# Performance work log

Measured on AMD Instinct MI355X. Metric: run time of the kernel, lower is better.

The kernel has to match this reference:

```python
import jax, jax.numpy as jnp
import numpy as np

B, N, D, H = 256, 196, 384, 1536  # batch, patches, dim, mlp hidden


def fake_quant(w, bits):
    """Symmetric per-tensor uniform fake quantization with straight-through estimator."""
    qmax = 2.0 ** (bits - 1) - 1.0
    scale = jnp.maximum(jnp.max(jnp.abs(w)) / qmax, 1e-8)
    q = jnp.clip(jnp.round(w / scale), -qmax, qmax) * scale
    return w + jax.lax.stop_gradient(q - w)


def setup_inputs() -> dict:
    key = jax.random.key(0)
    ks = jax.random.split(key, 8)
    return {
        "x": jax.random.normal(ks[0], (B, N, D), jnp.float32),
        "alpha1": jnp.ones((D,), jnp.float32),
        "beta1": jnp.zeros((D,), jnp.float32),
        "W_attn": jax.random.normal(ks[1], (N, N), jnp.float32) * (1.0 / np.sqrt(N)),
        "b_attn": jnp.zeros((N,), jnp.float32),
        "gamma1": jax.random.uniform(ks[2], (D,), jnp.float32) * 0.1,
        "alpha2": jnp.ones((D,), jnp.float32),
        "beta2": jnp.zeros((D,), jnp.float32),
        "W1": jax.random.normal(ks[3], (H, D), jnp.float32) * (1.0 / np.sqrt(D)),
        "b1": jnp.zeros((H,), jnp.float32),
        "W2": jax.random.normal(ks[4], (D, H), jnp.float32) * (1.0 / np.sqrt(H)),
        "b2": jnp.zeros((D,), jnp.float32),
        "gamma2": jax.random.uniform(ks[5], (D,), jnp.float32) * 0.1,
        "bits": 8,
    }


def reference(x, alpha1, beta1, W_attn, b_attn, gamma1,
              alpha2, beta2, W1, b1, W2, b2, gamma2, bits):
    # --- token-mixing branch ---
    org = x
    h = alpha1 * x + beta1                                   # Aff norm1, [B,N,D]
    # transpose(1,2) -> [B,D,N]; Linear(N,N); transpose back == einsum over patch dim
    Wq = fake_quant(W_attn, bits)
    h = jnp.einsum('bnd,mn->bmd', h, Wq) + b_attn[:, None]   # [B,N,D], bias per patch
    x = gamma1 * h + org                                     # layerscale + residual
    # --- channel-mixing branch ---
    org = x
    h = alpha2 * x + beta2                                   # Aff norm2
    h = jax.nn.gelu(h @ fake_quant(W1, bits).T + b1)         # [B,N,H]
    h = h @ fake_quant(W2, bits).T + b2                      # [B,N,D]
    return gamma2 * h + org
```

## Files before the change

kernel.cpp:

```cpp
#include <hip/hip_runtime.h>
#include <hip/hip_bf16.h>
#include <stdint.h>

#define Bb 256
#define Nn 196
#define Dd 384
#define Hh 1536
#define NPAD 224
#define MPAD 256
#define TTOT (Bb*Nn)
#define XLD 232

typedef __attribute__((ext_vector_type(8))) __bf16 bf16x8;
typedef __attribute__((ext_vector_type(4))) float f32x4;

#define GLD16(gp, lp) __builtin_amdgcn_global_load_lds( \
    (const __attribute__((address_space(1))) void*)(gp), \
    (__attribute__((address_space(3))) void*)(lp), 16, 0, 0)

__device__ __forceinline__ ushort f2bf(float f){
  union { float f; unsigned u; } v; v.f = f;
  unsigned r = v.u + 0x7FFFu + ((v.u >> 16) & 1u);
  return (ushort)(r >> 16);
}

__global__ void absmax_k(const float* __restrict__ w, int n, unsigned* __restrict__ out){
  float m = 0.f;
  for (int i = blockIdx.x*blockDim.x + threadIdx.x; i < n; i += gridDim.x*blockDim.x)
    m = fmaxf(m, fabsf(w[i]));
  #pragma unroll
  for (int o = 32; o >= 1; o >>= 1) m = fmaxf(m, __shfl_xor(m, o));
  __shared__ float sm[4];
  if ((threadIdx.x & 63) == 0) sm[threadIdx.x >> 6] = m;
  __syncthreads();
  if (threadIdx.x == 0){
    float mm = fmaxf(fmaxf(sm[0], sm[1]), fmaxf(sm[2], sm[3]));
    atomicMax(out, __float_as_uint(mm));
  }
}

__global__ void quant_attn_k(const float* __restrict__ W, const unsigned* __restrict__ amax,
                             const int* __restrict__ bitsp, ushort* __restrict__ Wq){
  int idx = blockIdx.x*256 + threadIdx.x;
  int m = idx / NPAD, n = idx - m*NPAD;
  float qmax = (float)((1 << (bitsp[0]-1)) - 1);
  float s = fmaxf(__uint_as_float(amax[0]) / qmax, 1e-8f);
  float v = 0.f;
  if (m < Nn && n < Nn){
    float q = fminf(fmaxf(rintf(W[m*Nn + n] / s), -qmax), qmax);
    v = q * s;
  }
  Wq[idx] = f2bf(v);
}

__global__ void quant_k(const float* __restrict__ W, int n, const unsigned* __restrict__ amax,
                        const int* __restrict__ bitsp, ushort* __restrict__ Wq){
  int idx = blockIdx.x*256 + threadIdx.x;
  if (idx >= n) return;
  float qmax = (float)((1 << (bitsp[0]-1)) - 1);
  float s = fmaxf(__uint_as_float(amax[0]) / qmax, 1e-8f);
  float q = fminf(fmaxf(rintf(W[idx] / s), -qmax), qmax);
  Wq[idx] = f2bf(q * s);
}

__device__ __forceinline__ void stage_tile(const ushort* __restrict__ src, long ld, int k0,
                                           ushort* dst){
  const int tid = threadIdx.x;
  const long row = tid >> 2;
  const int  c8  = (tid & 3) * 8;
  GLD16(src + row*ld + k0 + c8,        dst + tid*8);
  GLD16(src + (row+64)*ld + k0 + c8,   dst + 2048 + tid*8);
}

__device__ __forceinline__ void gemm_core_gl(const ushort* __restrict__ A, long ldA,
                                             const ushort* __restrict__ B, long ldB,
                                             int K, ushort* As, ushort* Bs, f32x4 acc[4][4]){
  const int tid  = threadIdx.x;
  const int lane = tid & 63;
  const int wr   = (tid >> 7) & 1;
  const int wc   = (tid >> 6) & 1;
  const int arow = lane & 15;
  const int koff = (lane >> 4) * 8;
  for (int k0 = 0; k0 < K; k0 += 32){
    __syncthreads();
    stage_tile(A, ldA, k0, As);
    stage_tile(B, ldB, k0, Bs);
    __syncthreads();
    bf16x8 ag[4], bg[4];
    #pragma unroll
    for (int i=0;i<4;i++){
      ag[i] = *(const bf16x8*)&As[(wr*64 + i*16 + arow)*32 + koff];
      bg[i] = *(const bf16x8*)&Bs[(wc*64 + i*16 + arow)*32 + koff];
    }
    #pragma unroll
    for (int i=0;i<4;i++)
      #pragma unroll
      for (int j=0;j<4;j++)
        acc[i][j] = __builtin_amdgcn_mfma_f32_16x16x32_bf16(ag[i], bg[j], acc[i][j], 0, 0, 0);
  }
}

__global__ __launch_bounds__(256) void gemm1_k(const ushort* __restrict__ Wq,
    const float* __restrict__ x,
    const float* __restrict__ alpha1, const float* __restrict__ beta1,
    const float* __restrict__ b_attn, const float* __restrict__ gamma1,
    const float* __restrict__ alpha2, const float* __restrict__ beta2,
    float* __restrict__ x1, ushort* __restrict__ hn2){
  __shared__ ushort Xs[128*XLD];
  __shared__ ushort BufAs[8192];
  const int tid = threadIdx.x;
  const int b = blockIdx.y, dt = blockIdx.x, d0 = dt*128;

  {
    float* buf = (float*)BufAs;
    const int dme = tid & 127;
    const float a1 = alpha1[d0 + dme], be1 = beta1[d0 + dme];
    for (int p = 0; p < 7; p++){
      __syncthreads();
      #pragma unroll
      for (int c = 0; c < 4; c++){
        int nn = p*32 + c*8 + (tid >> 5);
        int ncl = nn < Nn ? nn : Nn - 1;
        GLD16(x + ((long)b*Nn + ncl)*Dd + d0 + (tid & 31)*4,
              (char*)BufAs + c*4096 + tid*16);
      }
      __syncthreads();
      for (int g = tid >> 7; g < 4; g += 2){
        int n0 = g*8;
        ushort o[8];
        #pragma unroll
        for (int t = 0; t < 8; t++){
          int na = p*32 + n0 + t;
          float val = (na < Nn) ? fmaf(a1, buf[(n0 + t)*128 + dme], be1) : 0.f;
          o[t] = f2bf(val);
        }
        *(int4*)&Xs[dme*XLD + p*32 + n0] = *(int4*)o;
      }
    }
  }

  const int lane = tid & 63;
  const int wr = (tid >> 7) & 1, wc = (tid >> 6) & 1;
  const int arow = lane & 15, koff = (lane >> 4)*8;
  ushort* As = BufAs;
  for (int mt = 0; mt < 2; mt++){
    f32x4 acc[4][4] = {};
    const ushort* Wt = Wq + (long)mt*128*NPAD;
    for (int k0 = 0; k0 < NPAD; k0 += 32){
      __syncthreads();
      stage_tile(Wt, NPAD, k0, As);
      __syncthreads();
      bf16x8 ag[4], bg[4];
      #pragma unroll
      for (int i=0;i<4;i++){
        ag[i] = *(const bf16x8*)&As[(wr*64 + i*16 + arow)*32 + koff];
        bg[i] = *(const bf16x8*)&Xs[(wc*64 + i*16 + arow)*XLD + k0 + koff];
      }
      #pragma unroll
      for (int i=0;i<4;i++)
        #pragma unroll
        for (int j=0;j<4;j++)
          acc[i][j] = __builtin_amdgcn_mfma_f32_16x16x32_bf16(ag[i], bg[j], acc[i][j], 0, 0, 0);
    }
    #pragma unroll
    for (int i=0;i<4;i++){
      #pragma unroll
      for (int j=0;j<4;j++){
        int d = d0 + wc*64 + j*16 + (lane & 15);
        float g1 = gamma1[d], a2 = alpha2[d], b2v = beta2[d];
        #pragma unroll
        for (int r=0;r<4;r++){
          int m = mt*128 + wr*64 + i*16 + (lane >> 4)*4 + r;
          if (m < Nn){
            long idx = ((long)b*Nn + m)*Dd + d;
            float o = fmaf(g1, acc[i][j][r] + b_attn[m], x[idx]);
            x1[idx]  = o;
            hn2[idx] = f2bf(fmaf(a2, o, b2v));
          }
        }
      }
    }
  }
}

__global__ __launch_bounds__(256) void gemm2_k(const ushort* __restrict__ hn2,
    const ushort* __restrict__ W1q, const float* __restrict__ b1,
    ushort* __restrict__ h2, int t0){
  __shared__ ushort As[4096];
  __shared__ ushort Bs[4096];
  int ht = blockIdx.x, tt = blockIdx.y;
  f32x4 acc[4][4] = {};
  gemm_core_gl(hn2 + ((long)t0 + tt*128)*Dd, Dd, W1q + (long)ht*128*Dd, Dd, Dd, As, Bs, acc);
  int lane = threadIdx.x & 63;
  int wr = (threadIdx.x >> 7) & 1, wc = (threadIdx.x >> 6) & 1;
  #pragma unroll
  for (int i=0;i<4;i++){
    #pragma unroll
    for (int j=0;j<4;j++){
      int h = ht*128 + wc*64 + j*16 + (lane & 15);
      float bias = b1[h];
      #pragma unroll
      for (int r=0;r<4;r++){
        int t = tt*128 + wr*64 + i*16 + (lane >> 4)*4 + r;
        float v = acc[i][j][r] + bias;
        float u = 0.7978845608028654f * v * fmaf(0.044715f, v*v, 1.f);
        float g = v / (1.f + __expf(-2.f*u));
        h2[(long)t*Hh + h] = f2bf(g);
      }
    }
  }
}

__global__ __launch_bounds__(256) void gemm3_k(const ushort* __restrict__ h2,
    const ushort* __restrict__ W2q, const float* __restrict__ b2,
    const float* __restrict__ gamma2, float* __restrict__ out, int t0){
  __shared__ ushort As[4096];
  __shared__ ushort Bs[4096];
  int dt = blockIdx.x, tt = blockIdx.y;
  f32x4 acc[4][4] = {};
  gemm_core_gl(h2 + (long)tt*128*Hh, Hh, W2q + (long)dt*128*Hh, Hh, Hh, As, Bs, acc);
  int lane = threadIdx.x & 63;
  int wr = (threadIdx.x >> 7) & 1, wc = (threadIdx.x >> 6) & 1;
  #pragma unroll
  for (int i=0;i<4;i++){
    #pragma unroll
    for (int j=0;j<4;j++){
      int d = dt*128 + wc*64 + j*16 + (lane & 15);
      float g2 = gamma2[d], bias = b2[d];
      #pragma unroll
      for (int r=0;r<4;r++){
        long t = (long)t0 + tt*128 + wr*64 + i*16 + (lane >> 4)*4 + r;
        long idx = t*Dd + d;
        out[idx] = fmaf(g2, acc[i][j][r] + bias, out[idx]);
      }
    }
  }
}

extern "C" void kernel_launch(void* const* d_in, const int* in_sizes, int n_in,
                              void* d_out, int out_size, void* d_ws, size_t ws_size,
                              hipStream_t stream){
  const float* x      = (const float*)d_in[0];
  const float* alpha1 = (const float*)d_in[1];
  const float* beta1  = (const float*)d_in[2];
  const float* W_attn = (const float*)d_in[3];
  const float* b_attn = (const float*)d_in[4];
  const float* gamma1 = (const float*)d_in[5];
  const float* alpha2 = (const float*)d_in[6];
  const float* beta2  = (const float*)d_in[7];
  const float* W1     = (const float*)d_in[8];
  const float* b1     = (const float*)d_in[9];
  const float* W2     = (const float*)d_in[10];
  const float* b2     = (const float*)d_in[11];
  const float* gamma2 = (const float*)d_in[12];
  const int*   bits   = (const int*)d_in[13];

  char* ws = (char*)d_ws;
  unsigned* amax = (unsigned*)ws;
  ushort* Wq   = (ushort*)(ws + 256);
  ushort* W1q  = (ushort*)(ws + 114944);
  ushort* W2q  = (ushort*)(ws + 1294592);
  ushort* hn2  = (ushort*)(ws + 2474240);
  ushort* h2   = (ushort*)(ws + 41009408);
  float*  x1   = (float*)d_out;

  const size_t fixed_end = 41009408ull;
  int nchunk;
  if      (ws_size >= fixed_end + 154140672ull) nchunk = 1;
  else if (ws_size >= fixed_end +  77070336ull) nchunk = 2;
  else                                          nchunk = 4;
  const int TC = TTOT / nchunk;

  hipMemsetAsync(amax, 0, 256, stream);
  absmax_k<<<128, 256, 0, stream>>>(W_attn, Nn*Nn, amax + 0);
  absmax_k<<<256, 256, 0, stream>>>(W1, Hh*Dd, amax + 1);
  absmax_k<<<256, 256, 0, stream>>>(W2, Hh*Dd, amax + 2);
  quant_attn_k<<<(MPAD*NPAD)/256, 256, 0, stream>>>(W_attn, amax, bits, Wq);
  quant_k<<<(Hh*Dd)/256, 256, 0, stream>>>(W1, Hh*Dd, amax + 1, bits, W1q);
  quant_k<<<(Hh*Dd)/256, 256, 0, stream>>>(W2, Hh*Dd, amax + 2, bits, W2q);
  gemm1_k<<<dim3(3, Bb), 256, 0, stream>>>(Wq, x, alpha1, beta1, b_attn, gamma1,
                                           alpha2, beta2, x1, hn2);
  for (int c = 0; c < nchunk; c++){
    gemm2_k<<<dim3(Hh/128, TC/128), 256, 0, stream>>>(hn2, W1q, b1, h2, c*TC);
    gemm3_k<<<dim3(Dd/128, TC/128), 256, 0, stream>>>(h2, W2q, b2, gamma2,
                                                      (float*)d_out, c*TC);
  }
}
```

Before: 401.5 us.

## Fuse MLP up-projection, GELU and down-projection into one kernel

Replaces the separate gemm2 and gemm3 kernels, and the chunked hidden-activation buffer between them, with a single fused MLP kernel. Each block owns 64 tokens and loops over 12 hidden slices of 128. For each slice it computes the first GEMM, applies GELU into a swizzled LDS tile, and accumulates that tile into the 384-wide output accumulator. This removes the write and re-read of the 50176x1536 bf16 hidden tensor in global memory and drops the extra launches. In exchange, all of W1 and W2 is restreamed per 64-token block, tiles are smaller with many syncthreads, and register pressure from 96 output accumulators may limit occupancy.

New measurement: 437.8 us. 1.09x slower.

```diff
diff --git a/kernel.cpp b/kernel.cpp
--- a/kernel.cpp
+++ b/kernel.cpp
@@ -10,6 +10,7 @@
 #define MPAD 256
 #define TTOT (Bb*Nn)
 #define XLD 232
+#define TK 64
 
 typedef __attribute__((ext_vector_type(8))) __bf16 bf16x8;
 typedef __attribute__((ext_vector_type(4))) float f32x4;
@@ -72,34 +73,6 @@
   GLD16(src + (row+64)*ld + k0 + c8,   dst + 2048 + tid*8);
 }
 
-__device__ __forceinline__ void gemm_core_gl(const ushort* __restrict__ A, long ldA,
-                                             const ushort* __restrict__ B, long ldB,
-                                             int K, ushort* As, ushort* Bs, f32x4 acc[4][4]){
-  const int tid  = threadIdx.x;
-  const int lane = tid & 63;
-  const int wr   = (tid >> 7) & 1;
-  const int wc   = (tid >> 6) & 1;
-  const int arow = lane & 15;
-  const int koff = (lane >> 4) * 8;
-  for (int k0 = 0; k0 < K; k0 += 32){
-    __syncthreads();
-    stage_tile(A, ldA, k0, As);
-    stage_tile(B, ldB, k0, Bs);
-    __syncthreads();
-    bf16x8 ag[4], bg[4];
-    #pragma unroll
-    for (int i=0;i<4;i++){
-      ag[i] = *(const bf16x8*)&As[(wr*64 + i*16 + arow)*32 + koff];
-      bg[i] = *(const bf16x8*)&Bs[(wc*64 + i*16 + arow)*32 + koff];
-    }
-    #pragma unroll
-    for (int i=0;i<4;i++)
-      #pragma unroll
-      for (int j=0;j<4;j++)
-        acc[i][j] = __builtin_amdgcn_mfma_f32_16x16x32_bf16(ag[i], bg[j], acc[i][j], 0, 0, 0);
-  }
-}
-
 __global__ __launch_bounds__(256) void gemm1_k(const ushort* __restrict__ Wq,
     const float* __restrict__ x,
     const float* __restrict__ alpha1, const float* __restrict__ beta1,
@@ -183,55 +156,105 @@
   }
 }
 
-__global__ __launch_bounds__(256) void gemm2_k(const ushort* __restrict__ hn2,
-    const ushort* __restrict__ W1q, const float* __restrict__ b1,
-    ushort* __restrict__ h2, int t0){
-  __shared__ ushort As[4096];
-  __shared__ ushort Bs[4096];
-  int ht = blockIdx.x, tt = blockIdx.y;
-  f32x4 acc[4][4] = {};
-  gemm_core_gl(hn2 + ((long)t0 + tt*128)*Dd, Dd, W1q + (long)ht*128*Dd, Dd, Dd, As, Bs, acc);
-  int lane = threadIdx.x & 63;
-  int wr = (threadIdx.x >> 7) & 1, wc = (threadIdx.x >> 6) & 1;
+__global__ __launch_bounds__(256, 2) void mlp_k(const ushort* __restrict__ hn2,
+    const ushort* __restrict__ W1q, const ushort* __restrict__ W2q,
+    const float* __restrict__ b1, const float* __restrict__ b2,
+    const float* __restrict__ gamma2, float* __restrict__ out){
+  __shared__ ushort As[TK*32];
+  __shared__ ushort Ws[384*32];
+  __shared__ ushort Ps[TK*128];
+  const int tid  = threadIdx.x;
+  const int lane = tid & 63;
+  const int wave = tid >> 6;
+  const int wr   = wave >> 1;
+  const int wc   = wave & 1;
+  const int wd   = wave * 96;
+  const int arow = lane & 15;
+  const int koff = (lane >> 4) * 8;
+  const long t0  = (long)blockIdx.x * TK;
+  const int  c8  = (tid & 3) * 8;
+  const int  srow = tid >> 2;
+
+  f32x4 oacc[4][6] = {};
+
+  for (int hs = 0; hs < 12; hs++){
+    f32x4 pacc[2][4] = {};
+    const ushort* W1s = W1q + (long)hs*128*Dd;
+    for (int k0 = 0; k0 < Dd; k0 += 32){
+      __syncthreads();
+      GLD16(hn2 + (t0 + srow)*Dd + k0 + c8, As + tid*8);
+      GLD16(W1s + (long)srow*Dd + k0 + c8,      Ws + tid*8);
+      GLD16(W1s + (long)(srow+64)*Dd + k0 + c8, Ws + 2048 + tid*8);
+      __syncthreads();
+      bf16x8 ag[2], bg[4];
+      #pragma unroll
+      for (int i=0;i<2;i++) ag[i] = *(const bf16x8*)&As[(wr*32 + i*16 + arow)*32 + koff];
+      #pragma unroll
+      for (int j=0;j<4;j++) bg[j] = *(const bf16x8*)&Ws[(wc*64 + j*16 + arow)*32 + koff];
+      #pragma unroll
+      for (int i=0;i<2;i++)
+        #pragma unroll
+        for (int j=0;j<4;j++)
+          pacc[i][j] = __builtin_amdgcn_mfma_f32_16x16x32_bf16(ag[i], bg[j], pacc[i][j], 0, 0, 0);
+    }
+    {
+      float b1v[4];
+      #pragma unroll
+      for (int j=0;j<4;j++) b1v[j] = b1[hs*128 + wc*64 + j*16 + (lane & 15)];
+      #pragma unroll
+      for (int i=0;i<2;i++){
+        #pragma unroll
+        for (int j=0;j<4;j++){
+          int hcol = wc*64 + j*16 + (lane & 15);
+          #pragma unroll
+          for (int r=0;r<4;r++){
+            int row = wr*32 + i*16 + (lane >> 4)*4 + r;
+            float v = pacc[i][j][r] + b1v[j];
+            float u = 0.7978845608028654f * v * fmaf(0.044715f, v*v, 1.f);
+            float g = v / (1.f + __expf(-2.f*u));
+            Ps[row*128 + (hcol ^ ((row & 7) << 3))] = f2bf(g);
+          }
+        }
+      }
+    }
+    for (int k0 = 0; k0 < 128; k0 += 32){
+      __syncthreads();
+      #pragma unroll
+      for (int q=0;q<6;q++)
+        GLD16(W2q + (long)(q*64 + srow)*Hh + hs*128 + k0 + c8, Ws + q*2048 + tid*8);
+      __syncthreads();
+      bf16x8 pa[4], bg[6];
+      #pragma unroll
+      for (int i=0;i<4;i++){
+        int row = i*16 + arow;
+        pa[i] = *(const bf16x8*)&Ps[row*128 + ((k0 + koff) ^ ((row & 7) << 3))];
+      }
+      #pragma unroll
+      for (int j=0;j<6;j++) bg[j] = *(const bf16x8*)&Ws[(wd + j*16 + arow)*32 + koff];
+      #pragma unroll
+      for (int i=0;i<4;i++)
+        #pragma unroll
+        for (int j=0;j<6;j++)
+          oacc[i][j] = __builtin_amdgcn_mfma_f32_16x16x32_bf16(pa[i], bg[j], oacc[i][j], 0, 0, 0);
+    }
+  }
+
+  float g2v[6], b2v[6];
+  #pragma unroll
+  for (int j=0;j<6;j++){
+    int d = wd + j*16 + (lane & 15);
+    g2v[j] = gamma2[d]; b2v[j] = b2[d];
+  }
   #pragma unroll
   for (int i=0;i<4;i++){
     #pragma unroll
-    for (int j=0;j<4;j++){
-      int h = ht*128 + wc*64 + j*16 + (lane & 15);
-      float bias = b1[h];
+    for (int j=0;j<6;j++){
+      int d = wd + j*16 + (lane & 15);
       #pragma unroll
       for (int r=0;r<4;r++){
-        int t = tt*128 + wr*64 + i*16 + (lane >> 4)*4 + r;
-        float v = acc[i][j][r] + bias;
-        float u = 0.7978845608028654f * v * fmaf(0.044715f, v*v, 1.f);
-        float g = v / (1.f + __expf(-2.f*u));
-        h2[(long)t*Hh + h] = f2bf(g);
-      }
-    }
-  }
-}
-
-__global__ __launch_bounds__(256) void gemm3_k(const ushort* __restrict__ h2,
-    const ushort* __restrict__ W2q, const float* __restrict__ b2,
-    const float* __restrict__ gamma2, float* __restrict__ out, int t0){
-  __shared__ ushort As[4096];
-  __shared__ ushort Bs[4096];
-  int dt = blockIdx.x, tt = blockIdx.y;
-  f32x4 acc[4][4] = {};
-  gemm_core_gl(h2 + (long)tt*128*Hh, Hh, W2q + (long)dt*128*Hh, Hh, Hh, As, Bs, acc);
-  int lane = threadIdx.x & 63;
-  int wr = (threadIdx.x >> 7) & 1, wc = (threadIdx.x >> 6) & 1;
-  #pragma unroll
-  for (int i=0;i<4;i++){
-    #pragma unroll
-    for (int j=0;j<4;j++){
-      int d = dt*128 + wc*64 + j*16 + (lane & 15);
-      float g2 = gamma2[d], bias = b2[d];
-      #pragma unroll
-      for (int r=0;r<4;r++){
-        long t = (long)t0 + tt*128 + wr*64 + i*16 + (lane >> 4)*4 + r;
+        long t = t0 + i*16 + (lane >> 4)*4 + r;
         long idx = t*Dd + d;
-        out[idx] = fmaf(g2, acc[i][j][r] + bias, out[idx]);
+        out[idx] = fmaf(g2v[j], oacc[i][j][r] + b2v[j], out[idx]);
       }
     }
   }
@@ -261,15 +284,7 @@
   ushort* W1q  = (ushort*)(ws + 114944);
   ushort* W2q  = (ushort*)(ws + 1294592);
   ushort* hn2  = (ushort*)(ws + 2474240);
-  ushort* h2   = (ushort*)(ws + 41009408);
   float*  x1   = (float*)d_out;
-
-  const size_t fixed_end = 41009408ull;
-  int nchunk;
-  if      (ws_size >= fixed_end + 154140672ull) nchunk = 1;
-  else if (ws_size >= fixed_end +  77070336ull) nchunk = 2;
-  else                                          nchunk = 4;
-  const int TC = TTOT / nchunk;
 
   hipMemsetAsync(amax, 0, 256, stream);
   absmax_k<<<128, 256, 0, stream>>>(W_attn, Nn*Nn, amax + 0);
@@ -280,9 +295,5 @@
   quant_k<<<(Hh*Dd)/256, 256, 0, stream>>>(W2, Hh*Dd, amax + 2, bits, W2q);
   gemm1_k<<<dim3(3, Bb), 256, 0, stream>>>(Wq, x, alpha1, beta1, b_attn, gamma1,
                                            alpha2, beta2, x1, hn2);
-  for (int c = 0; c < nchunk; c++){
-    gemm2_k<<<dim3(Hh/128, TC/128), 256, 0, stream>>>(hn2, W1q, b1, h2, c*TC);
-    gemm3_k<<<dim3(Dd/128, TC/128), 256, 0, stream>>>(h2, W2q, b2, gamma2,
-                                                      (float*)d_out, c*TC);
-  }
-}
+  mlp_k<<<TTOT/TK, 256, 0, stream>>>(hn2, W1q, W2q, b1, b2, gamma2, (float*)d_out);
+}
```
